# Optimization experiments

Measured on AMD Instinct MI355X. Metric: run time of the kernel, lower is better.

Reference implementation:

```python
import jax, jax.numpy as jnp
import numpy as np

V, BS, E, H, L, FC = 50257, 1024, 768, 12, 6, 4
B, T = 4, 1024
HS = E // H
FF = FC * E
EPS = 1e-5


def setup_inputs() -> dict:
    key = jax.random.key(0)
    ks = jax.random.split(key, 24)
    s = 0.02
    inp = {
        'idx': jax.random.randint(ks[0], (B, T), 0, V),
        'targets': jax.random.randint(ks[1], (B, T), 0, V),
        'tok_emb': jax.random.normal(ks[2], (V, E), jnp.float32) * s,
        'pos_emb': jax.random.normal(ks[3], (BS, E), jnp.float32) * s,
        'Wq': jax.random.normal(ks[4], (L, H, E, HS), jnp.float32) * s,
        'Wk': jax.random.normal(ks[5], (L, H, E, HS), jnp.float32) * s,
        'Wv': jax.random.normal(ks[6], (L, H, E, HS), jnp.float32) * s,
        'Wo': jax.random.normal(ks[7], (L, E, E), jnp.float32) * s,
        'bo': jnp.zeros((L, E), jnp.float32),
        'ln1_s': jnp.ones((L, E), jnp.float32),
        'ln1_b': jnp.zeros((L, E), jnp.float32),
        'ln2_s': jnp.ones((L, E), jnp.float32),
        'ln2_b': jnp.zeros((L, E), jnp.float32),
        'W1': jax.random.normal(ks[8], (L, E, FF), jnp.float32) * s,
        'b1': jnp.zeros((L, FF), jnp.float32),
        'W2': jax.random.normal(ks[9], (L, FF, E), jnp.float32) * s,
        'b2': jnp.zeros((L, E), jnp.float32),
        'lnf_s': jnp.ones((E,), jnp.float32),
        'lnf_b': jnp.zeros((E,), jnp.float32),
        'Wlm': jax.random.normal(ks[10], (E, V), jnp.float32) * s,
        'blm': jnp.zeros((V,), jnp.float32),
    }
    return inp


def _ln(x, scale, bias):
    mu = x.mean(-1, keepdims=True)
    var = ((x - mu) ** 2).mean(-1, keepdims=True)
    return (x - mu) * jax.lax.rsqrt(var + EPS) * scale + bias


def _forward(idx, targets, tok_emb, pos_emb, Wq, Wk, Wv, Wo, bo,
             ln1_s, ln1_b, ln2_s, ln2_b, W1, b1, W2, b2,
             lnf_s, lnf_b, Wlm, blm):
    Bc, Tc = idx.shape
    x = tok_emb[idx] + pos_emb[:Tc]                      # [B,T,E]
    causal = jnp.tril(jnp.ones((Tc, Tc), bool))          # [T,T]

    def block(x, p):
        wq, wk, wv, wo_, bo_, l1s, l1b, l2s, l2b, w1, b1_, w2, b2_ = p
        h = _ln(x, l1s, l1b)
        q = jnp.einsum('bte,hed->bhtd', h, wq)
        k = jnp.einsum('bte,hed->bhtd', h, wk)
        v = jnp.einsum('bte,hed->bhtd', h, wv)
        scores = jnp.einsum('bhtd,bhsd->bhts', q, k) * (HS ** -0.5)
        scores = jnp.where(causal, scores, -jnp.inf)
        att = jax.nn.softmax(scores, axis=-1)            # [B,H,T,T]
        o = jnp.einsum('bhts,bhsd->bhtd', att, v)
        o = o.transpose(0, 2, 1, 3).reshape(Bc, Tc, E)   # concat heads
        x = x + jnp.einsum('bte,ef->btf', o, wo_) + bo_
        h2 = _ln(x, l2s, l2b)
        f = jax.nn.relu(jnp.einsum('bte,ef->btf', h2, w1) + b1_)
        x = x + jnp.einsum('btf,fe->bte', f, w2) + b2_
        return x, None

    layers = (Wq, Wk, Wv, Wo, bo, ln1_s, ln1_b, ln2_s, ln2_b, W1, b1, W2, b2)
    x, _ = jax.lax.scan(block, x, layers)
    x = _ln(x, lnf_s, lnf_b)
    logits = jnp.einsum('bte,ev->btv', x, Wlm) + blm     # [B,T,V]
    logp = jax.nn.log_softmax(logits, axis=-1)
    nll = -jnp.take_along_axis(logp, targets[..., None], axis=-1)[..., 0]
    loss = nll.mean()
    return logits, loss


def reference(idx, targets, tok_emb, pos_emb, Wq, Wk, Wv, Wo, bo,
              ln1_s, ln1_b, ln2_s, ln2_b, W1, b1, W2, b2,
              lnf_s, lnf_b, Wlm, blm):
    return _forward(idx, targets, tok_emb, pos_emb, Wq, Wk, Wv, Wo, bo,
                    ln1_s, ln1_b, ln2_s, ln2_b, W1, b1, W2, b2,
                    lnf_s, lnf_b, Wlm, blm)
```

## Files before the change

### kernel.cpp

```cpp
#include <hip/hip_runtime.h>
#include <hip/hip_bf16.h>
#include <cstdint>
#include <cstddef>

#define NB 4
#define NT 1024
#define NE 768
#define NH 12
#define NHS 64
#define NL 6
#define NFF 3072
#define NV 50257
#define NVP 50304
#define NTOK (NB*NT)
#define NCB_LM (NVP/128)
#define QKVS 2304

typedef __attribute__((ext_vector_type(8))) short short8;
typedef __attribute__((ext_vector_type(4))) float f32x4;
typedef __hip_bfloat16 bf16;

__global__ __launch_bounds__(256) void embed_kernel(
    const int* __restrict__ idx, const float* __restrict__ tok,
    const float* __restrict__ pos, float* __restrict__ x)
{
  int bt = blockIdx.x;
  int token = idx[bt];
  int t = bt & (NT - 1);
  const float* tr = tok + (size_t)token * NE;
  const float* pr = pos + (size_t)t * NE;
  float* xr = x + (size_t)bt * NE;
  for (int i = threadIdx.x; i < NE; i += 256)
    xr[i] = tr[i] + pr[i];
}

__global__ __launch_bounds__(256) void ln_kernel(
    const float* __restrict__ in, const float* __restrict__ sc,
    const float* __restrict__ bi, bf16* __restrict__ out)
{
  int row = blockIdx.x, tid = threadIdx.x;
  const float* xr = in + (size_t)row * NE;
  float v0 = xr[tid], v1 = xr[tid + 256], v2 = xr[tid + 512];
  float s = v0 + v1 + v2;
  float ss = v0 * v0 + v1 * v1 + v2 * v2;
  #pragma unroll
  for (int o = 32; o > 0; o >>= 1) {
    s  += __shfl_xor(s, o);
    ss += __shfl_xor(ss, o);
  }
  __shared__ float r1[4], r2[4];
  if ((tid & 63) == 0) { r1[tid >> 6] = s; r2[tid >> 6] = ss; }
  __syncthreads();
  float tot = r1[0] + r1[1] + r1[2] + r1[3];
  float tss = r2[0] + r2[1] + r2[2] + r2[3];
  float mu  = tot * (1.f / NE);
  float var = tss * (1.f / NE) - mu * mu;
  float rs  = rsqrtf(var + 1e-5f);
  bf16* orow = out + (size_t)row * NE;
  orow[tid]       = __float2bfloat16((v0 - mu) * rs * sc[tid]       + bi[tid]);
  orow[tid + 256] = __float2bfloat16((v1 - mu) * rs * sc[tid + 256] + bi[tid + 256]);
  orow[tid + 512] = __float2bfloat16((v2 - mu) * rs * sc[tid + 512] + bi[tid + 512]);
}

__global__ __launch_bounds__(256) void tconv_kernel(
    const float* __restrict__ src, bf16* __restrict__ dst,
    int R, int Cs, int Cd, int zdiv,
    size_t srcZstr, size_t dstLstr, size_t dstHstr)
{
  __shared__ float t[32][33];
  int z = blockIdx.z;
  int l = z / zdiv, h = z - l * zdiv;
  src += (size_t)z * srcZstr;
  dst += (size_t)l * dstLstr + (size_t)h * dstHstr;
  int c0 = blockIdx.x * 32, r0 = blockIdx.y * 32;
  int tx = threadIdx.x & 31, ty = threadIdx.x >> 5;
  #pragma unroll
  for (int i = 0; i < 32; i += 8) {
    int r = r0 + ty + i, c = c0 + tx;
    t[ty + i][tx] = (c < Cs) ? src[(size_t)r * Cs + c] : 0.f;
  }
  __syncthreads();
  #pragma unroll
  for (int i = 0; i < 32; i += 8) {
    int c = c0 + ty + i, r = r0 + tx;
    if (c < Cd) dst[(size_t)c * R + r] = __float2bfloat16(t[tx][ty + i]);
  }
}

template<int MREP, bool SWZ>
__global__ __launch_bounds__(256) void gemm_bf(
    const bf16* __restrict__ A,
    const bf16* __restrict__ BT,
    float* __restrict__ Cf, bf16* __restrict__ Cbf,
    const float* __restrict__ bias, const float* __restrict__ Rres,
    float* __restrict__ ps,
    int M, int N, int K, int relu, int ncb)
{
  constexpr int BMT = MREP * 32;
  __shared__ bf16 As[BMT][64];
  __shared__ bf16 Bs[128][64];
  __shared__ float ps2[BMT][2];
  int tid = threadIdx.x;
  int lane = tid & 63;
  int w = __builtin_amdgcn_readfirstlane(tid >> 6);
  int wr = w >> 1, wc = w & 1;
  int cb = blockIdx.x;
  int row0 = blockIdx.y * BMT;
  int col0 = cb * 128;

  f32x4 acc[MREP][4] = {};

  for (int k0 = 0; k0 < K; k0 += 64) {
    #pragma unroll
    for (int r = 0; r < MREP; ++r) {
      int c = r * 256 + tid;
      int trow = c >> 3;
      int schunk = SWZ ? ((c & 7) ^ (trow & 7)) : (c & 7);
      const bf16* ga = A + (size_t)(row0 + trow) * K + k0 + (schunk << 3);
      __builtin_amdgcn_global_load_lds(
          (const __attribute__((address_space(1))) void*)ga,
          (__attribute__((address_space(3))) void*)((char*)&As[0][0] + (unsigned)c * 16),
          16, 0, 0);
    }
    #pragma unroll
    for (int r = 0; r < 4; ++r) {
      int c = r * 256 + tid;
      int trow = c >> 3;
      int schunk = SWZ ? ((c & 7) ^ (trow & 7)) : (c & 7);
      const bf16* gb = BT + (size_t)(col0 + trow) * K + k0 + (schunk << 3);
      __builtin_amdgcn_global_load_lds(
          (const __attribute__((address_space(1))) void*)gb,
          (__attribute__((address_space(3))) void*)((char*)&Bs[0][0] + (unsigned)c * 16),
          16, 0, 0);
    }
    __syncthreads();
    int l15 = lane & 15;
    int g8 = (lane >> 4) << 3;
    int sx = SWZ ? ((l15 & 7) << 3) : 0;
    #pragma unroll
    for (int kk = 0; kk < 64; kk += 32) {
      short8 a[MREP], b[4];
      #pragma unroll
      for (int m = 0; m < MREP; ++m)
        a[m] = *(const short8*)&As[wr * (MREP * 16) + m * 16 + l15][(kk + g8) ^ sx];
      #pragma unroll
      for (int n = 0; n < 4; ++n)
        b[n] = *(const short8*)&Bs[wc * 64 + n * 16 + l15][(kk + g8) ^ sx];
      #pragma unroll
      for (int m = 0; m < MREP; ++m)
        #pragma unroll
        for (int n = 0; n < 4; ++n)
          acc[m][n] = __builtin_amdgcn_mfma_f32_16x16x32_bf16(a[m], b[n], acc[m][n], 0, 0, 0);
    }
    __syncthreads();
  }

  int cr = lane >> 4;
  int cc = lane & 15;
  #pragma unroll
  for (int m = 0; m < MREP; ++m) {
    #pragma unroll
    for (int n = 0; n < 4; ++n) {
      int col = col0 + wc * 64 + n * 16 + cc;
      if (col >= N) continue;
      float bv = bias ? bias[col] : 0.f;
      #pragma unroll
      for (int e = 0; e < 4; ++e) {
        int row = row0 + wr * (MREP * 16) + m * 16 + cr * 4 + e;
        float v = acc[m][n][e] + bv;
        size_t off = (size_t)row * N + col;
        if (Rres) v += Rres[off];
        if (relu) v = fmaxf(v, 0.f);
        if (Cf)  Cf[off] = v;
        if (Cbf) Cbf[off] = __float2bfloat16(v);
      }
    }
  }

  if (ps) {
    #pragma unroll
    for (int m = 0; m < MREP; ++m) {
      #pragma unroll
      for (int e = 0; e < 4; ++e) {
        float ssum = 0.f;
        #pragma unroll
        for (int n = 0; n < 4; ++n) {
          int col = col0 + wc * 64 + n * 16 + cc;
          float val = (col < N) ? (acc[m][n][e] + (bias ? bias[col] : 0.f)) : -1e30f;
          ssum += __expf(val);
        }
        ssum += __shfl_xor(ssum, 1);
        ssum += __shfl_xor(ssum, 2);
        ssum += __shfl_xor(ssum, 4);
        ssum += __shfl_xor(ssum, 8);
        if (cc == 0) {
          int rl = wr * (MREP * 16) + m * 16 + cr * 4 + e;
          ps2[rl][wc] = ssum;
        }
      }
    }
    __syncthreads();
    for (int i = tid; i < MREP * 32; i += 256) {
      size_t o = (size_t)(row0 + i) * ncb + cb;
      ps[o] = ps2[i][0] + ps2[i][1];
    }
  }
}

#define LBK 32
__global__ __launch_bounds__(256) void lm_gemm(
    const bf16* __restrict__ A, const bf16* __restrict__ BT,
    float* __restrict__ Cf, const float* __restrict__ bias,
    float* __restrict__ ps, int M, int N, int K, int ncb)
{
  __shared__ bf16 As[2][128][LBK];
  __shared__ bf16 Bs[2][128][LBK];
  __shared__ float ps2[128][2];
  int tid = threadIdx.x;
  int lane = tid & 63;
  int w = __builtin_amdgcn_readfirstlane(tid >> 6);
  int wr = w >> 1, wc = w & 1;
  int row0 = blockIdx.y * 128, col0 = blockIdx.x * 128;
  int l15 = lane & 15;
  int g8 = (lane >> 4) << 3;

  f32x4 acc[4][4] = {};
  const int nk = K / LBK;

#define LM_STAGE(b, k0)                                                        \
  {                                                                            \
    _Pragma("unroll")                                                          \
    for (int r = 0; r < 2; ++r) {                                              \
      int c = r * 256 + tid;                                                   \
      int trow = c >> 2, tcol = (c & 3) << 3;                                  \
      const bf16* ga = A + (size_t)(row0 + trow) * K + (k0) + tcol;            \
      __builtin_amdgcn_global_load_lds(                                        \
          (const __attribute__((address_space(1))) void*)ga,                   \
          (__attribute__((address_space(3))) void*)((char*)&As[b][0][0] + (unsigned)c * 16), \
          16, 0, 0);                                                           \
    }                                                                          \
    _Pragma("unroll")                                                          \
    for (int r = 0; r < 2; ++r) {                                              \
      int c = r * 256 + tid;                                                   \
      int trow = c >> 2, tcol = (c & 3) << 3;                                  \
      const bf16* gb = BT + (size_t)(col0 + trow) * K + (k0) + tcol;           \
      __builtin_amdgcn_global_load_lds(                                        \
          (const __attribute__((address_space(1))) void*)gb,                   \
          (__attribute__((address_space(3))) void*)((char*)&Bs[b][0][0] + (unsigned)c * 16), \
          16, 0, 0);                                                           \
    }                                                                          \
  }

  LM_STAGE(0, 0);
  asm volatile("s_waitcnt vmcnt(0)" ::: "memory");
  __builtin_amdgcn_s_barrier();

  int cur = 0;
  for (int t = 0; t < nk - 1; ++t) {
    LM_STAGE(cur ^ 1, (t + 1) * LBK);
    short8 a[4], bb[4];
    #pragma unroll
    for (int m = 0; m < 4; ++m)
      a[m] = *(const short8*)&As[cur][wr * 64 + m * 16 + l15][g8];
    #pragma unroll
    for (int n = 0; n < 4; ++n)
      bb[n] = *(const short8*)&Bs[cur][wc * 64 + n * 16 + l15][g8];
    #pragma unroll
    for (int m = 0; m < 4; ++m)
      #pragma unroll
      for (int n = 0; n < 4; ++n)
        acc[m][n] = __builtin_amdgcn_mfma_f32_16x16x32_bf16(a[m], bb[n], acc[m][n], 0, 0, 0);
    asm volatile("s_waitcnt vmcnt(0)" ::: "memory");
    __builtin_amdgcn_s_barrier();
    cur ^= 1;
  }
  {
    short8 a[4], bb[4];
    #pragma unroll
    for (int m = 0; m < 4; ++m)
      a[m] = *(const short8*)&As[cur][wr * 64 + m * 16 + l15][g8];
    #pragma unroll
    for (int n = 0; n < 4; ++n)
      bb[n] = *(const short8*)&Bs[cur][wc * 64 + n * 16 + l15][g8];
    #pragma unroll
    for (int m = 0; m < 4; ++m)
      #pragma unroll
      for (int n = 0; n < 4; ++n)
        acc[m][n] = __builtin_amdgcn_mfma_f32_16x16x32_bf16(a[m], bb[n], acc[m][n], 0, 0, 0);
  }

  int cr = lane >> 4;
  int cc = lane & 15;
  #pragma unroll
  for (int m = 0; m < 4; ++m) {
    #pragma unroll
    for (int n = 0; n < 4; ++n) {
      int col = col0 + wc * 64 + n * 16 + cc;
      if (col >= N) continue;
      float bv = bias[col];
      #pragma unroll
      for (int e = 0; e < 4; ++e) {
        int row = row0 + wr * 64 + m * 16 + cr * 4 + e;
        Cf[(size_t)row * N + col] = acc[m][n][e] + bv;
      }
    }
  }

  #pragma unroll
  for (int m = 0; m < 4; ++m) {
    #pragma unroll
    for (int e = 0; e < 4; ++e) {
      float ssum = 0.f;
      #pragma unroll
      for (int n = 0; n < 4; ++n) {
        int col = col0 + wc * 64 + n * 16 + cc;
        float val = (col < N) ? (acc[m][n][e] + bias[col]) : -1e30f;
        ssum += __expf(val);
      }
      ssum += __shfl_xor(ssum, 1);
      ssum += __shfl_xor(ssum, 2);
      ssum += __shfl_xor(ssum, 4);
      ssum += __shfl_xor(ssum, 8);
      if (cc == 0) {
        int rl = wr * 64 + m * 16 + cr * 4 + e;
        ps2[rl][wc] = ssum;
      }
    }
  }
  __syncthreads();
  for (int i = tid; i < 128; i += 256) {
    size_t o = (size_t)(row0 + i) * ncb + blockIdx.x;
    ps[o] = ps2[i][0] + ps2[i][1];
  }
#undef LM_STAGE
}

static __device__ inline unsigned short bfbits(float x) {
  bf16 h = __float2bfloat16(x);
  return *reinterpret_cast<unsigned short*>(&h);
}

__global__ __launch_bounds__(256) void fattn_kernel(
    const bf16* __restrict__ QKV, bf16* __restrict__ O)
{
  __shared__ unsigned short Ks[64][72];
  __shared__ unsigned short Vt[64][72];
  __shared__ unsigned short Pl[4][16][72];
  int qt = blockIdx.x, h = blockIdx.y, b = blockIdx.z;
  int tid = threadIdx.x;
  int lane = tid & 63;
  int w = tid >> 6;
  int l15 = lane & 15, g = lane >> 4;
  int brow = b * NT;
  int qbase = qt * 64;
  int q_loc = w * 16 + l15;

  short8 bq[2];
  {
    const bf16* qp = QKV + (size_t)(brow + qbase + q_loc) * QKVS + h * 64 + g * 8;
    bq[0] = *(const short8*)qp;
    bq[1] = *(const short8*)(qp + 32);
  }

  float m_run = -1e30f, l_run = 0.f;
  f32x4 acc[4] = {};

  for (int kt = 0; kt <= qt; ++kt) {
    int s0 = kt * 64;
    #pragma unroll
    for (int i = 0; i < 2; ++i) {
      int c = tid + i * 256;
      int row = c >> 3, colg = (c & 7) * 8;
      const bf16* kp = QKV + (size_t)(brow + s0 + row) * QKVS + NE + h * 64 + colg;
      const bf16* vp = QKV + (size_t)(brow + s0 + row) * QKVS + 2 * NE + h * 64 + colg;
      short8 kv = *(const short8*)kp;
      short8 vv = *(const short8*)vp;
      *(short8*)&Ks[row][colg] = kv;
      #pragma unroll
      for (int j = 0; j < 8; ++j)
        Vt[colg + j][row] = (unsigned short)vv[j];
    }
    __syncthreads();

    f32x4 sf[4] = {};
    #pragma unroll
    for (int kk = 0; kk < 2; ++kk) {
      #pragma unroll
      for (int m = 0; m < 4; ++m) {
        short8 a = *(const short8*)&Ks[m * 16 + l15][kk * 32 + g * 8];
        sf[m] = __builtin_amdgcn_mfma_f32_16x16x32_bf16(a, bq[kk], sf[m], 0, 0, 0);
      }
    }

    float sv[4][4];
    float mx = -1e30f;
    bool diag = (kt == qt);
    #pragma unroll
    for (int m = 0; m < 4; ++m)
      #pragma unroll
      for (int e = 0; e < 4; ++e) {
        float v = sf[m][e] * 0.125f;
        if (diag) {
          int sl = m * 16 + g * 4 + e;
          if (sl > q_loc) v = -1e30f;
        }
        sv[m][e] = v;
        mx = fmaxf(mx, v);
      }
    mx = fmaxf(mx, __shfl_xor(mx, 16));
    mx = fmaxf(mx, __shfl_xor(mx, 32));
    float m_new = fmaxf(m_run, mx);
    float p[4][4];
    float rs = 0.f;
    #pragma unroll
    for (int m = 0; m < 4; ++m)
      #pragma unroll
      for (int e = 0; e < 4; ++e) {
        float pe = __expf(sv[m][e] - m_new);
        p[m][e] = pe;
        rs += pe;
      }
    rs += __shfl_xor(rs, 16);
    rs += __shfl_xor(rs, 32);
    float sc_old = __expf(m_run - m_new);
    l_run = l_run * sc_old + rs;
    m_run = m_new;
    #pragma unroll
    for (int dm = 0; dm < 4; ++dm)
      #pragma unroll
      for (int e = 0; e < 4; ++e)
        acc[dm][e] *= sc_old;

    #pragma unroll
    for (int m = 0; m < 4; ++m)
      #pragma unroll
      for (int ep = 0; ep < 2; ++ep) {
        unsigned u = (unsigned)bfbits(p[m][2 * ep]) |
                     ((unsigned)bfbits(p[m][2 * ep + 1]) << 16);
        *(unsigned*)&Pl[w][l15][m * 16 + g * 4 + ep * 2] = u;
      }

    #pragma unroll
    for (int ks = 0; ks < 2; ++ks) {
      short8 pb = *(const short8*)&Pl[w][l15][ks * 32 + g * 8];
      #pragma unroll
      for (int dm = 0; dm < 4; ++dm) {
        short8 av = *(const short8*)&Vt[dm * 16 + l15][ks * 32 + g * 8];
        acc[dm] = __builtin_amdgcn_mfma_f32_16x16x32_bf16(av, pb, acc[dm], 0, 0, 0);
      }
    }
    __syncthreads();
  }

  float inv = 1.f / l_run;
  bf16* op = O + (size_t)(brow + qbase + q_loc) * NE + h * 64;
  #pragma unroll
  for (int dm = 0; dm < 4; ++dm)
    #pragma unroll
    for (int ep = 0; ep < 2; ++ep) {
      int d = dm * 16 + g * 4 + ep * 2;
      unsigned u = (unsigned)bfbits(acc[dm][2 * ep] * inv) |
                   ((unsigned)bfbits(acc[dm][2 * ep + 1] * inv) << 16);
      *(unsigned*)((unsigned short*)op + d) = u;
    }
}

__global__ __launch_bounds__(128) void nll_finish(
    const float* __restrict__ ps,
    const float* __restrict__ logits, const int* __restrict__ targets,
    float* __restrict__ nll)
{
  int row = blockIdx.x, tid = threadIdx.x;
  float s = 0.f;
  for (int i = tid; i < NCB_LM; i += 128)
    s += ps[(size_t)row * NCB_LM + i];
  #pragma unroll
  for (int o = 32; o > 0; o >>= 1) s += __shfl_xor(s, o);
  __shared__ float ss[2];
  if ((tid & 63) == 0) ss[tid >> 6] = s;
  __syncthreads();
  if (tid == 0) {
    float S = ss[0] + ss[1];
    float tgt = logits[(size_t)row * NV + targets[row]];
    nll[row] = logf(S) - tgt;
  }
}

__global__ __launch_bounds__(256) void loss_kernel(
    const float* __restrict__ nll, float* __restrict__ out)
{
  int tid = threadIdx.x;
  float s = 0.f;
  for (int i = tid; i < NTOK; i += 256) s += nll[i];
  #pragma unroll
  for (int o = 32; o > 0; o >>= 1) s += __shfl_xor(s, o);
  __shared__ float red[4];
  if ((tid & 63) == 0) red[tid >> 6] = s;
  __syncthreads();
  if (tid == 0) out[0] = (red[0] + red[1] + red[2] + red[3]) * (1.f / NTOK);
}

static inline void gemm(const bf16* A, const bf16* BT,
                        float* Cf, bf16* Cbf,
                        const float* bias, const float* Rres, float* ps,
                        int M, int N, int Npad, int K, int relu,
                        int mrep, hipStream_t st)
{
  int ncb = Npad / 128;
  dim3 g(ncb, M / (mrep * 32));
  if (mrep == 4)
    gemm_bf<4, true><<<g, dim3(256), 0, st>>>(A, BT, Cf, Cbf, bias, Rres, ps, M, N, K, relu, ncb);
  else
    gemm_bf<2, true><<<g, dim3(256), 0, st>>>(A, BT, Cf, Cbf, bias, Rres, ps, M, N, K, relu, ncb);
}

extern "C" void kernel_launch(void* const* d_in, const int* in_sizes, int n_in,
                              void* d_out, int out_size, void* d_ws, size_t ws_size,
                              hipStream_t stream)
{
  const int*   idx     = (const int*)  d_in[0];
  const int*   targets = (const int*)  d_in[1];
  const float* tok_emb = (const float*)d_in[2];
  const float* pos_emb = (const float*)d_in[3];
  const float* Wq      = (const float*)d_in[4];
  const float* Wk      = (const float*)d_in[5];
  const float* Wv      = (const float*)d_in[6];
  const float* Wo      = (const float*)d_in[7];
  const float* bo      = (const float*)d_in[8];
  const float* ln1_s   = (const float*)d_in[9];
  const float* ln1_b   = (const float*)d_in[10];
  const float* ln2_s   = (const float*)d_in[11];
  const float* ln2_b   = (const float*)d_in[12];
  const float* W1      = (const float*)d_in[13];
  const float* b1      = (const float*)d_in[14];
  const float* W2      = (const float*)d_in[15];
  const float* b2      = (const float*)d_in[16];
  const float* lnf_s   = (const float*)d_in[17];
  const float* lnf_b   = (const float*)d_in[18];
  const float* Wlm     = (const float*)d_in[19];
  const float* blm     = (const float*)d_in[20];
  float* out = (float*)d_out;

  const size_t XE = (size_t)NTOK * NE;
  char* p = (char*)d_ws;
  float* x     = (float*)p;         p += XE * 4;
  bf16* h_bf   = (bf16*)p;          p += XE * 2;
  bf16* qkv_bf = (bf16*)p;          p += (size_t)NTOK * QKVS * 2;
  bf16* att_bf = (bf16*)p;          p += XE * 2;
  bf16* f_bf   = (bf16*)p;          p += (size_t)NTOK * NFF * 2;
  bf16* wqkv_a = (bf16*)p;          p += (size_t)NL * QKVS * NE * 2;
  bf16* wto_a  = (bf16*)p;          p += (size_t)NL * NE * NE * 2;
  bf16* wt1_a  = (bf16*)p;          p += (size_t)NL * NFF * NE * 2;
  bf16* wt2_a  = (bf16*)p;          p += (size_t)NL * NE * NFF * 2;
  bf16* wtlm   = (bf16*)p;          p += (size_t)NVP * NE * 2;
  float* psb   = (float*)p;         p += (size_t)NTOK * NCB_LM * 4;
  float* nll   = (float*)p;         p += (size_t)NTOK * 4;

  embed_kernel<<<dim3(NTOK), dim3(256), 0, stream>>>(idx, tok_emb, pos_emb, x);

  tconv_kernel<<<dim3(2, 24, NL * NH), dim3(256), 0, stream>>>(
      Wq, wqkv_a, NE, NHS, NHS, NH,
      (size_t)NE * NHS, (size_t)QKVS * NE, (size_t)NHS * NE);
  tconv_kernel<<<dim3(2, 24, NL * NH), dim3(256), 0, stream>>>(
      Wk, wqkv_a + (size_t)NE * NE, NE, NHS, NHS, NH,
      (size_t)NE * NHS, (size_t)QKVS * NE, (size_t)NHS * NE);
  tconv_kernel<<<dim3(2, 24, NL * NH), dim3(256), 0, stream>>>(
      Wv, wqkv_a + (size_t)2 * NE * NE, NE, NHS, NHS, NH,
      (size_t)NE * NHS, (size_t)QKVS * NE, (size_t)NHS * NE);
  tconv_kernel<<<dim3(24, 24, NL), dim3(256), 0, stream>>>(
      Wo, wto_a, NE, NE, NE, 1, (size_t)NE * NE, (size_t)NE * NE, 0);
  tconv_kernel<<<dim3(96, 24, NL), dim3(256), 0, stream>>>(
      W1, wt1_a, NE, NFF, NFF, 1, (size_t)NE * NFF, (size_t)NFF * NE, 0);
  tconv_kernel<<<dim3(24, 96, NL), dim3(256), 0, stream>>>(
      W2, wt2_a, NFF, NE, NE, 1, (size_t)NFF * NE, (size_t)NE * NFF, 0);
  tconv_kernel<<<dim3(NVP / 32, 24, 1), dim3(256), 0, stream>>>(
      Wlm, wtlm, NE, NV, NVP, 1, 0, 0, 0);

  for (int l = 0; l < NL; ++l) {
    ln_kernel<<<dim3(NTOK), dim3(256), 0, stream>>>(x, ln1_s + l*NE, ln1_b + l*NE, h_bf);

    gemm(h_bf, wqkv_a + (size_t)l * QKVS * NE, nullptr, qkv_bf, nullptr, nullptr, nullptr,
         NTOK, QKVS, QKVS, NE, 0, 4, stream);

    fattn_kernel<<<dim3(NT / 64, NH, NB), dim3(256), 0, stream>>>(qkv_bf, att_bf);

    gemm(att_bf, wto_a + (size_t)l * NE * NE, x, nullptr, bo + l*NE, x, nullptr,
         NTOK, NE, NE, NE, 0, 2, stream);

    ln_kernel<<<dim3(NTOK), dim3(256), 0, stream>>>(x, ln2_s + l*NE, ln2_b + l*NE, h_bf);

    gemm(h_bf, wt1_a + (size_t)l * NFF * NE, nullptr, f_bf, b1 + l*NFF, nullptr, nullptr,
         NTOK, NFF, NFF, NE, 1, 4, stream);
    gemm(f_bf, wt2_a + (size_t)l * NE * NFF, x, nullptr, b2 + l*NE, x, nullptr,
         NTOK, NE, NE, NFF, 0, 2, stream);
  }

  ln_kernel<<<dim3(NTOK), dim3(256), 0, stream>>>(x, lnf_s, lnf_b, h_bf);

  {
    dim3 g(NCB_LM, NTOK / 128);
    lm_gemm<<<g, dim3(256), 0, stream>>>(h_bf, wtlm, out, blm, psb,
                                         NTOK, NV, NE, NCB_LM);
  }

  nll_finish<<<dim3(NTOK), dim3(128), 0, stream>>>(psb, out, targets, nll);
  loss_kernel<<<dim3(1), dim3(256), 0, stream>>>(nll, out + (size_t)NTOK * NV);
}
```

Before: 2.170 ms.

## Make LM-head GEMM blocks loop over row bands with continuous prefetch

```diff
diff --git a/kernel.cpp b/kernel.cpp
--- a/kernel.cpp
+++ b/kernel.cpp
@@ -208,10 +208,13 @@
 }
 
 #define LBK 32
+#define LMK 768
+#define NKSTEP (LMK / LBK)
+#define NBAND 8
 __global__ __launch_bounds__(256) void lm_gemm(
     const bf16* __restrict__ A, const bf16* __restrict__ BT,
     float* __restrict__ Cf, const float* __restrict__ bias,
-    float* __restrict__ ps, int M, int N, int K, int ncb)
+    float* __restrict__ ps, int M, int N, int ncb)
 {
   __shared__ bf16 As[2][128][LBK];
   __shared__ bf16 Bs[2][128][LBK];
@@ -220,20 +223,24 @@
   int lane = tid & 63;
   int w = __builtin_amdgcn_readfirstlane(tid >> 6);
   int wr = w >> 1, wc = w & 1;
-  int row0 = blockIdx.y * 128, col0 = blockIdx.x * 128;
+  int col0 = blockIdx.x * 128;
+  int band0 = blockIdx.y * NBAND;
   int l15 = lane & 15;
   int g8 = (lane >> 4) << 3;
+  int cr = lane >> 4;
+  int cc = lane & 15;
 
   f32x4 acc[4][4] = {};
-  const int nk = K / LBK;
-
-#define LM_STAGE(b, k0)                                                        \
+
+#define LM_STAGE(b, band, t)                                                   \
   {                                                                            \
+    int row0s = (band0 + (band)) * 128;                                        \
+    int k0 = (t) * LBK;                                                        \
     _Pragma("unroll")                                                          \
     for (int r = 0; r < 2; ++r) {                                              \
       int c = r * 256 + tid;                                                   \
       int trow = c >> 2, tcol = (c & 3) << 3;                                  \
-      const bf16* ga = A + (size_t)(row0 + trow) * K + (k0) + tcol;            \
+      const bf16* ga = A + (size_t)(row0s + trow) * LMK + k0 + tcol;           \
       __builtin_amdgcn_global_load_lds(                                        \
           (const __attribute__((address_space(1))) void*)ga,                   \
           (__attribute__((address_space(3))) void*)((char*)&As[b][0][0] + (unsigned)c * 16), \
@@ -243,7 +250,7 @@
     for (int r = 0; r < 2; ++r) {                                              \
       int c = r * 256 + tid;                                                   \
       int trow = c >> 2, tcol = (c & 3) << 3;                                  \
-      const bf16* gb = BT + (size_t)(col0 + trow) * K + (k0) + tcol;           \
+      const bf16* gb = BT + (size_t)(col0 + trow) * LMK + k0 + tcol;           \
       __builtin_amdgcn_global_load_lds(                                        \
           (const __attribute__((address_space(1))) void*)gb,                   \
           (__attribute__((address_space(3))) void*)((char*)&Bs[b][0][0] + (unsigned)c * 16), \
@@ -251,86 +258,82 @@
     }                                                                          \
   }
 
-  LM_STAGE(0, 0);
+  LM_STAGE(0, 0, 0);
   asm volatile("s_waitcnt vmcnt(0)" ::: "memory");
   __builtin_amdgcn_s_barrier();
 
   int cur = 0;
-  for (int t = 0; t < nk - 1; ++t) {
-    LM_STAGE(cur ^ 1, (t + 1) * LBK);
-    short8 a[4], bb[4];
-    #pragma unroll
-    for (int m = 0; m < 4; ++m)
-      a[m] = *(const short8*)&As[cur][wr * 64 + m * 16 + l15][g8];
-    #pragma unroll
-    for (int n = 0; n < 4; ++n)
-      bb[n] = *(const short8*)&Bs[cur][wc * 64 + n * 16 + l15][g8];
-    #pragma unroll
-    for (int m = 0; m < 4; ++m)
+  int sband = 0, st = 1;
+  for (int band = 0; band < NBAND; ++band) {
+    for (int t = 0; t < NKSTEP; ++t) {
+      bool last = (band == NBAND - 1) && (t == NKSTEP - 1);
+      if (!last) {
+        LM_STAGE(cur ^ 1, sband, st);
+        if (++st == NKSTEP) { st = 0; ++sband; }
+      }
+      short8 a[4], bb[4];
+      #pragma unroll
+      for (int m = 0; m < 4; ++m)
+        a[m] = *(const short8*)&As[cur][wr * 64 + m * 16 + l15][g8];
       #pragma unroll
       for (int n = 0; n < 4; ++n)
-        acc[m][n] = __builtin_amdgcn_mfma_f32_16x16x32_bf16(a[m], bb[n], acc[m][n], 0, 0, 0);
-    asm volatile("s_waitcnt vmcnt(0)" ::: "memory");
-    __builtin_amdgcn_s_barrier();
-    cur ^= 1;
-  }
-  {
-    short8 a[4], bb[4];
-    #pragma unroll
-    for (int m = 0; m < 4; ++m)
-      a[m] = *(const short8*)&As[cur][wr * 64 + m * 16 + l15][g8];
-    #pragma unroll
-    for (int n = 0; n < 4; ++n)
-      bb[n] = *(const short8*)&Bs[cur][wc * 64 + n * 16 + l15][g8];
-    #pragma unroll
-    for (int m = 0; m < 4; ++m)
-      #pragma unroll
-      for (int n = 0; n < 4; ++n)
-        acc[m][n] = __builtin_amdgcn_mfma_f32_16x16x32_bf16(a[m], bb[n], acc[m][n], 0, 0, 0);
-  }
-
-  int cr = lane >> 4;
-  int cc = lane & 15;
-  #pragma unroll
-  for (int m = 0; m < 4; ++m) {
-    #pragma unroll
-    for (int n = 0; n < 4; ++n) {
-      int col = col0 + wc * 64 + n * 16 + cc;
-      if (col >= N) continue;
-      float bv = bias[col];
-      #pragma unroll
-      for (int e = 0; e < 4; ++e) {
-        int row = row0 + wr * 64 + m * 16 + cr * 4 + e;
-        Cf[(size_t)row * N + col] = acc[m][n][e] + bv;
-      }
-    }
-  }
-
-  #pragma unroll
-  for (int m = 0; m < 4; ++m) {
-    #pragma unroll
-    for (int e = 0; e < 4; ++e) {
-      float ssum = 0.f;
-      #pragma unroll
-      for (int n = 0; n < 4; ++n) {
-        int col = col0 + wc * 64 + n * 16 + cc;
-        float val = (col < N) ? (acc[m][n][e] + bias[col]) : -1e30f;
-        ssum += __expf(val);
-      }
-      ssum += __shfl_xor(ssum, 1);
-      ssum += __shfl_xor(ssum, 2);
-      ssum += __shfl_xor(ssum, 4);
-      ssum += __shfl_xor(ssum, 8);
-      if (cc == 0) {
-        int rl = wr * 64 + m * 16 + cr * 4 + e;
-        ps2[rl][wc] = ssum;
-      }
-    }
-  }
-  __syncthreads();
-  for (int i = tid; i < 128; i += 256) {
-    size_t o = (size_t)(row0 + i) * ncb + blockIdx.x;
-    ps[o] = ps2[i][0] + ps2[i][1];
+        bb[n] = *(const short8*)&Bs[cur][wc * 64 + n * 16 + l15][g8];
+      #pragma unroll
+      for (int m = 0; m < 4; ++m)
+        #pragma unroll
+        for (int n = 0; n < 4; ++n)
+          acc[m][n] = __builtin_amdgcn_mfma_f32_16x16x32_bf16(a[m], bb[n], acc[m][n], 0, 0, 0);
+
+      if (t == NKSTEP - 1) {
+        int row0 = (band0 + band) * 128;
+        #pragma unroll
+        for (int m = 0; m < 4; ++m) {
+          #pragma unroll
+          for (int n = 0; n < 4; ++n) {
+            int col = col0 + wc * 64 + n * 16 + cc;
+            if (col >= N) continue;
+            float bv = bias[col];
+            #pragma unroll
+            for (int e = 0; e < 4; ++e) {
+              int row = row0 + wr * 64 + m * 16 + cr * 4 + e;
+              Cf[(size_t)row * N + col] = acc[m][n][e] + bv;
+            }
+          }
+        }
+        #pragma unroll
+        for (int m = 0; m < 4; ++m) {
+          #pragma unroll
+          for (int e = 0; e < 4; ++e) {
+            float ssum = 0.f;
+            #pragma unroll
+            for (int n = 0; n < 4; ++n) {
+              int col = col0 + wc * 64 + n * 16 + cc;
+              float val = (col < N) ? (acc[m][n][e] + bias[col]) : -1e30f;
+              ssum += __expf(val);
+            }
+            ssum += __shfl_xor(ssum, 1);
+            ssum += __shfl_xor(ssum, 2);
+            ssum += __shfl_xor(ssum, 4);
+            ssum += __shfl_xor(ssum, 8);
+            if (cc == 0) ps2[wr * 64 + m * 16 + cr * 4 + e][wc] = ssum;
+          }
+        }
+        __syncthreads();
+        for (int i = tid; i < 128; i += 256) {
+          size_t o = (size_t)(row0 + i) * ncb + blockIdx.x;
+          ps[o] = ps2[i][0] + ps2[i][1];
+        }
+        #pragma unroll
+        for (int m = 0; m < 4; ++m)
+          #pragma unroll
+          for (int n = 0; n < 4; ++n)
+            acc[m][n] = f32x4{0.f, 0.f, 0.f, 0.f};
+      }
+
+      asm volatile("s_waitcnt vmcnt(0)" ::: "memory");
+      __builtin_amdgcn_s_barrier();
+      cur ^= 1;
+    }
   }
 #undef LM_STAGE
 }
@@ -598,9 +601,9 @@
   ln_kernel<<<dim3(NTOK), dim3(256), 0, stream>>>(x, lnf_s, lnf_b, h_bf);
 
   {
-    dim3 g(NCB_LM, NTOK / 128);
+    dim3 g(NCB_LM, NTOK / (NBAND * 128));
     lm_gemm<<<g, dim3(256), 0, stream>>>(h_bf, wtlm, out, blm, psb,
-                                         NTOK, NV, NE, NCB_LM);
+                                         NTOK, NV, NCB_LM);
   }
 
   nll_finish<<<dim3(NTOK), dim3(128), 0, stream>>>(psb, out, targets, nll);
```

Result: slower. 2.668 ms (+22.9%).
